# Kernel tuning notes

Hardware: AMD Instinct MI355X
Metric: run time of the kernel (lower is better)

The kernel has to match this reference:

```python
import jax, jax.numpy as jnp
import numpy as np

POOLED_H = 7
POOLED_W = 7
SAMPLING_RATIO = 2


def setup_inputs() -> dict:
    key = jax.random.key(0)
    k1, k2, k3, k4 = jax.random.split(key, 4)
    B, C, H, W = 2, 256, 192, 192
    N = 1024
    stride = 16
    img_h, img_w = H * stride, W * stride
    feature = jax.random.normal(k1, (B, C, H, W), dtype=jnp.float32)
    # well-formed rois: (batch_idx, x1, y1, x2, y2) in image coordinates
    bidx = jax.random.randint(k2, (N, 1), 0, B).astype(jnp.float32)
    p1 = jax.random.uniform(k3, (N, 2), minval=0.0, maxval=0.7)
    wh = jax.random.uniform(k4, (N, 2), minval=0.02, maxval=0.3)
    x1y1 = p1 * jnp.array([img_w, img_h], jnp.float32)
    x2y2 = jnp.minimum(x1y1 + wh * jnp.array([img_w, img_h], jnp.float32),
                       jnp.array([img_w - 1.0, img_h - 1.0], jnp.float32))
    rois = jnp.concatenate([bidx, x1y1[:, :1], x1y1[:, 1:], x2y2[:, :1], x2y2[:, 1:]], axis=1)
    return {"rois": rois, "feature": feature, "stride": stride}


def _roi_align(feature, rois, pooled_h, pooled_w, spatial_scale, ratio):
    B, C, H, W = feature.shape
    N = rois.shape[0]
    b = rois[:, 0].astype(jnp.int32)                     # [N]
    x1 = rois[:, 1] * spatial_scale
    y1 = rois[:, 2] * spatial_scale
    x2 = rois[:, 3] * spatial_scale
    y2 = rois[:, 4] * spatial_scale
    roi_w = jnp.maximum(x2 - x1, 1.0)                    # classic (non-aligned) RoIAlign
    roi_h = jnp.maximum(y2 - y1, 1.0)
    bin_w = roi_w / pooled_w
    bin_h = roi_h / pooled_h

    Sy, Sx = pooled_h * ratio, pooled_w * ratio
    iy = (jnp.arange(Sy, dtype=feature.dtype) + 0.5) / ratio  # in units of bin_h
    ix = (jnp.arange(Sx, dtype=feature.dtype) + 0.5) / ratio
    y = y1[:, None] + iy[None, :] * bin_h[:, None]       # [N, Sy]
    x = x1[:, None] + ix[None, :] * bin_w[:, None]       # [N, Sx]

    def interp_axis(c, size):
        valid = (c > -1.0) & (c < size)
        cc = jnp.clip(c, 0.0, size - 1)
        lo = jnp.floor(cc).astype(jnp.int32)
        lo = jnp.minimum(lo, size - 1)
        hi = jnp.minimum(lo + 1, size - 1)
        frac = cc - lo.astype(c.dtype)
        return valid, lo, hi, frac

    vy, y0, y1i, fy = interp_axis(y, H)
    vx, x0, x1i, fx = interp_axis(x, W)

    hy, ly = (1.0 - fy), fy                              # [N, Sy]
    hx, lx = (1.0 - fx), fx                              # [N, Sx]

    bI = b[:, None, None]

    def gather(yi, xi):
        # -> [N, Sy, Sx, C]
        return feature[bI, :, yi[:, :, None], xi[:, None, :]]

    val = (hy[:, :, None] * hx[:, None, :])[..., None] * gather(y0, x0) \
        + (hy[:, :, None] * lx[:, None, :])[..., None] * gather(y0, x1i) \
        + (ly[:, :, None] * hx[:, None, :])[..., None] * gather(y1i, x0) \
        + (ly[:, :, None] * lx[:, None, :])[..., None] * gather(y1i, x1i)
    val = val * (vy[:, :, None] & vx[:, None, :])[..., None].astype(val.dtype)

    # average sampling grid within each bin
    out = val.reshape(N, pooled_h, ratio, pooled_w, ratio, C).mean(axis=(2, 4))
    return out.transpose(0, 3, 1, 2)                     # [N, C, pooled_h, pooled_w]


def reference(rois, feature, stride):
    rois = rois[:, :5].astype(feature.dtype)
    spatial_scale = 1.0 / stride
    return _roi_align(feature, rois, POOLED_H, POOLED_W, spatial_scale, SAMPLING_RATIO)
```

## Files before the change

kernel.cpp:

```cpp
#include <hip/hip_runtime.h>
#include <hip/hip_fp16.h>

#define POOLED 7
#define RATIO 2

constexpr int C_ = 256;
constexpr int H_ = 192;
constexpr int W_ = 192;
constexpr int P_ = H_ * W_;
constexpr int PP2 = POOLED * POOLED;

constexpr int TC = 32;
constexpr int TP = 128;
constexpr int TPAD = TP + 1;

__global__ __launch_bounds__(256)
void nchw_to_nhwc_h(const float* __restrict__ in, __half* __restrict__ outT) {
    __shared__ float tile[TC][TPAD];
    const int b  = blockIdx.z;
    const int p0 = blockIdx.x * TP;
    const int c0 = blockIdx.y * TC;
    const float* src = in   + (size_t)b * C_ * P_;
    __half*      dst = outT + (size_t)b * P_ * C_;

    const int t = threadIdx.x;

    #pragma unroll
    for (int k = 0; k < 4; ++k) {
        const int q  = t + 256 * k;
        const int c  = q >> 5;
        const int pv = q & 31;
        const float4 v = *(const float4*)&src[(size_t)(c0 + c) * P_ + p0 + 4 * pv];
        tile[c][4 * pv + 0] = v.x;
        tile[c][4 * pv + 1] = v.y;
        tile[c][4 * pv + 2] = v.z;
        tile[c][4 * pv + 3] = v.w;
    }
    __syncthreads();

    #pragma unroll
    for (int k = 0; k < 2; ++k) {
        const int q  = t + 256 * k;
        const int p  = q >> 2;
        const int c8 = (q & 3) * 8;
        union { __half h[8]; float4 f; } u;
        #pragma unroll
        for (int i = 0; i < 8; ++i) u.h[i] = __float2half(tile[c8 + i][p]);
        *(float4*)&dst[(size_t)(p0 + p) * C_ + c0 + c8] = u.f;
    }
}

__global__ __launch_bounds__(512)
void roi_align_nhwc_h(const float* __restrict__ rois,
                      const __half* __restrict__ featT,
                      const int* __restrict__ stride_ptr,
                      float* __restrict__ out, int N) {
    constexpr int BSTRIDE = C_ + 2;
    __shared__ __half lds_out[PP2 * BSTRIDE];
    __shared__ int4 coord[28];

    const int n    = blockIdx.x;
    const int t    = threadIdx.x;
    const int lane = t & 63;
    const int wave = t >> 6;

    const float scale = 1.0f / (float)stride_ptr[0];
    const float* r = rois + (size_t)n * 5;
    const int   b   = (int)r[0];
    const float rx1 = r[1] * scale;
    const float ry1 = r[2] * scale;
    const float rx2 = r[3] * scale;
    const float ry2 = r[4] * scale;
    const float bin_w = fmaxf(rx2 - rx1, 1.0f) * (1.0f / (float)POOLED);
    const float bin_h = fmaxf(ry2 - ry1, 1.0f) * (1.0f / (float)POOLED);

    if (t < 28) {
        const bool  isY   = t < 14;
        const int   s     = isY ? t : t - 14;
        const float start = isY ? ry1 : rx1;
        const float bsz   = isY ? bin_h : bin_w;
        const int   size  = isY ? H_ : W_;
        const float cc0   = start + ((float)s + 0.5f) * 0.5f * bsz;
        const bool  valid = (cc0 > -1.0f) && (cc0 < (float)size);
        float cc = fminf(fmaxf(cc0, 0.0f), (float)(size - 1));
        int lo = (int)floorf(cc);
        if (lo > size - 1) lo = size - 1;
        const int hi = min(lo + 1, size - 1);
        const float frac = (cc - (float)lo) * 0.5f;
        int4 e;
        e.x = isY ? lo * W_ : lo;
        e.y = isY ? hi * W_ : hi;
        e.z = __float_as_int(frac);
        e.w = valid ? 1 : 0;
        coord[t] = e;
    }
    __syncthreads();

    const uint2* fbase = (const uint2*)featT + (size_t)b * P_ * (C_ / 4);
    const int cb = lane * 4;

    for (int bin = wave; bin < PP2; bin += 8) {
        const int ph = bin / POOLED;
        const int pw = bin - ph * POOLED;

        const int4 cxA = coord[14 + 2 * pw];
        const int4 cxB = coord[14 + 2 * pw + 1];

        __half2 acc01 = __float2half2_rn(0.f);
        __half2 acc23 = __float2half2_rn(0.f);

        #pragma unroll
        for (int sy = 0; sy < RATIO; ++sy) {
            const int4  cy = coord[2 * ph + sy];
            const float fy = __int_as_float(cy.z);
            const float hy = 0.5f - fy;

            #pragma unroll
            for (int sx = 0; sx < RATIO; ++sx) {
                const int4 cx = sx ? cxB : cxA;
                if (!(cy.w & cx.w)) continue;
                const float fx = __int_as_float(cx.z);
                const float hx = 0.5f - fx;

                const __half2 W00 = __float2half2_rn(hy * hx);
                const __half2 W01 = __float2half2_rn(hy * fx);
                const __half2 W10 = __float2half2_rn(fy * hx);
                const __half2 W11 = __float2half2_rn(fy * fx);

                const int p00 = cy.x + cx.x;
                const int p01 = cy.x + cx.y;
                const int p10 = cy.y + cx.x;
                const int p11 = cy.y + cx.y;

                const uint2 r00 = fbase[(size_t)p00 * (C_ / 4) + lane];
                const uint2 r01 = fbase[(size_t)p01 * (C_ / 4) + lane];
                const uint2 r10 = fbase[(size_t)p10 * (C_ / 4) + lane];
                const uint2 r11 = fbase[(size_t)p11 * (C_ / 4) + lane];

                acc01 = __hfma2(W00, *(const __half2*)&r00.x, acc01);
                acc23 = __hfma2(W00, *(const __half2*)&r00.y, acc23);
                acc01 = __hfma2(W01, *(const __half2*)&r01.x, acc01);
                acc23 = __hfma2(W01, *(const __half2*)&r01.y, acc23);
                acc01 = __hfma2(W10, *(const __half2*)&r10.x, acc01);
                acc23 = __hfma2(W10, *(const __half2*)&r10.y, acc23);
                acc01 = __hfma2(W11, *(const __half2*)&r11.x, acc01);
                acc23 = __hfma2(W11, *(const __half2*)&r11.y, acc23);
            }
        }

        __half2* dst = (__half2*)&lds_out[bin * BSTRIDE + cb];
        dst[0] = acc01;
        dst[1] = acc23;
    }

    __syncthreads();

    float4* o4 = (float4*)(out + (size_t)n * (C_ * PP2));
    for (int i = t; i < (C_ * PP2) / 4; i += 512) {
        const int l0 = i * 4;
        float4 v;
        #pragma unroll
        for (int j = 0; j < 4; ++j) {
            const int l  = l0 + j;
            const int c  = l / PP2;
            const int bn = l - c * PP2;
            ((float*)&v)[j] = __half2float(lds_out[bn * BSTRIDE + c]);
        }
        o4[i] = v;
    }
}

__global__ __launch_bounds__(256)
void roi_align_kernel(const float* __restrict__ rois,
                      const float* __restrict__ feat,
                      const int* __restrict__ stride_ptr,
                      int B, int C, int H, int W, int N,
                      float* __restrict__ out) {
    const int total = N * C * POOLED * POOLED;
    int idx = blockIdx.x * blockDim.x + threadIdx.x;
    if (idx >= total) return;

    const float scale = 1.0f / (float)stride_ptr[0];

    int pw = idx % POOLED;
    int ph = (idx / POOLED) % POOLED;
    int c  = (idx / (POOLED * POOLED)) % C;
    int n  = idx / (POOLED * POOLED * C);

    const float* r = rois + (size_t)n * 5;
    int b = (int)r[0];
    float x1 = r[1] * scale;
    float y1 = r[2] * scale;
    float x2 = r[3] * scale;
    float y2 = r[4] * scale;
    float bin_w = fmaxf(x2 - x1, 1.0f) / (float)POOLED;
    float bin_h = fmaxf(y2 - y1, 1.0f) / (float)POOLED;

    const float* plane = feat + ((size_t)b * C + c) * (size_t)(H * W);

    float acc = 0.0f;
    #pragma unroll
    for (int sy = 0; sy < RATIO; ++sy) {
        float iy = ((float)(ph * RATIO + sy) + 0.5f) / (float)RATIO;
        float yy = y1 + iy * bin_h;
        bool vy = (yy > -1.0f) && (yy < (float)H);
        float cy = fminf(fmaxf(yy, 0.0f), (float)(H - 1));
        int y0 = (int)floorf(cy);
        if (y0 > H - 1) y0 = H - 1;
        int y1i = min(y0 + 1, H - 1);
        float fy = cy - (float)y0;
        float hy = 1.0f - fy;

        #pragma unroll
        for (int sx = 0; sx < RATIO; ++sx) {
            float ix = ((float)(pw * RATIO + sx) + 0.5f) / (float)RATIO;
            float xx = x1 + ix * bin_w;
            bool vx = (xx > -1.0f) && (xx < (float)W);
            if (!(vy && vx)) continue;
            float cx = fminf(fmaxf(xx, 0.0f), (float)(W - 1));
            int x0 = (int)floorf(cx);
            if (x0 > W - 1) x0 = W - 1;
            int x1i = min(x0 + 1, W - 1);
            float fx = cx - (float)x0;
            float hx = 1.0f - fx;

            float v00 = plane[y0  * W + x0 ];
            float v01 = plane[y0  * W + x1i];
            float v10 = plane[y1i * W + x0 ];
            float v11 = plane[y1i * W + x1i];

            acc += hy * hx * v00 + hy * fx * v01 + fy * hx * v10 + fy * fx * v11;
        }
    }

    out[idx] = acc * 0.25f;
}

extern "C" void kernel_launch(void* const* d_in, const int* in_sizes, int n_in,
                              void* d_out, int out_size, void* d_ws, size_t ws_size,
                              hipStream_t stream) {
    const float* rois = (const float*)d_in[0];
    const float* feat = (const float*)d_in[1];
    const int* stride_ptr = (const int*)d_in[2];

    const int N = in_sizes[0] / 5;
    const int B = in_sizes[1] / (C_ * P_);
    float* out = (float*)d_out;

    const size_t need = (size_t)B * P_ * C_ * sizeof(__half);
    if (ws_size >= need) {
        __half* featT = (__half*)d_ws;
        dim3 tgrid(P_ / TP, C_ / TC, B);
        nchw_to_nhwc_h<<<tgrid, 256, 0, stream>>>(feat, featT);

        roi_align_nhwc_h<<<N, 512, 0, stream>>>(rois, featT, stride_ptr, out, N);
    } else {
        const int total = N * C_ * POOLED * POOLED;
        const int block = 256;
        const int grid = (total + block - 1) / block;
        roi_align_kernel<<<grid, block, 0, stream>>>(rois, feat, stride_ptr,
                                                     B, C_, H_, W_, N, out);
    }
}
```

Before: 165.6 us.

## Split RoIAlign across channel quarters with lane-parallel sample gathers and shuffle reduction

The RoI kernel now launches four 256-thread blocks per RoI, each owning a 64-channel slice, instead of one 512-thread block per RoI. Within a wave, the 8 lane groups each fetch one of the 8 bilinear corner/sample-x combinations as 16-byte loads, and the results are combined with xor-shuffles across groups. Each wave covers a contiguous range of bins and software-pipelines the next bin's loads ahead of the current bin's compute. The goal is more blocks for occupancy, wider memory transactions and better latency hiding, at the cost of shuffle-reduction work and only 8 lanes writing per bin.

```diff
diff --git a/kernel.cpp b/kernel.cpp
--- a/kernel.cpp
+++ b/kernel.cpp
@@ -50,16 +50,21 @@
     }
 }
 
-__global__ __launch_bounds__(512)
+constexpr int CB  = 64;
+constexpr int BPR = C_ / CB;
+constexpr int BST = CB + 2;
+
+__global__ __launch_bounds__(256, 8)
 void roi_align_nhwc_h(const float* __restrict__ rois,
                       const __half* __restrict__ featT,
                       const int* __restrict__ stride_ptr,
                       float* __restrict__ out, int N) {
-    constexpr int BSTRIDE = C_ + 2;
-    __shared__ __half lds_out[PP2 * BSTRIDE];
+    __shared__ __half lds_out[PP2 * BST];
     __shared__ int4 coord[28];
 
-    const int n    = blockIdx.x;
+    const int blk  = blockIdx.x;
+    const int n    = blk >> 2;
+    const int cq   = blk & 3;
     const int t    = threadIdx.x;
     const int lane = t & 63;
     const int wave = t >> 6;
@@ -96,67 +101,89 @@
     }
     __syncthreads();
 
-    const uint2* fbase = (const uint2*)featT + (size_t)b * P_ * (C_ / 4);
-    const int cb = lane * 4;
-
-    for (int bin = wave; bin < PP2; bin += 8) {
+    const uint4* fbase = (const uint4*)featT + (size_t)b * P_ * (C_ / 8);
+    const int cl4   = cq * (CB / 8) + (lane & 7);
+    const int g     = lane >> 3;
+    const int sxsel = g >> 2;
+    const int ysel  = (g >> 1) & 1;
+    const int xsel  = g & 1;
+
+    auto mkbin = [&](int bin, int& o0, int& o1, __half2& w0, __half2& w1) {
         const int ph = bin / POOLED;
         const int pw = bin - ph * POOLED;
-
-        const int4 cxA = coord[14 + 2 * pw];
-        const int4 cxB = coord[14 + 2 * pw + 1];
-
-        __half2 acc01 = __float2half2_rn(0.f);
-        __half2 acc23 = __float2half2_rn(0.f);
-
-        #pragma unroll
-        for (int sy = 0; sy < RATIO; ++sy) {
-            const int4  cy = coord[2 * ph + sy];
-            const float fy = __int_as_float(cy.z);
-            const float hy = 0.5f - fy;
-
-            #pragma unroll
-            for (int sx = 0; sx < RATIO; ++sx) {
-                const int4 cx = sx ? cxB : cxA;
-                if (!(cy.w & cx.w)) continue;
-                const float fx = __int_as_float(cx.z);
-                const float hx = 0.5f - fx;
-
-                const __half2 W00 = __float2half2_rn(hy * hx);
-                const __half2 W01 = __float2half2_rn(hy * fx);
-                const __half2 W10 = __float2half2_rn(fy * hx);
-                const __half2 W11 = __float2half2_rn(fy * fx);
-
-                const int p00 = cy.x + cx.x;
-                const int p01 = cy.x + cx.y;
-                const int p10 = cy.y + cx.x;
-                const int p11 = cy.y + cx.y;
-
-                const uint2 r00 = fbase[(size_t)p00 * (C_ / 4) + lane];
-                const uint2 r01 = fbase[(size_t)p01 * (C_ / 4) + lane];
-                const uint2 r10 = fbase[(size_t)p10 * (C_ / 4) + lane];
-                const uint2 r11 = fbase[(size_t)p11 * (C_ / 4) + lane];
-
-                acc01 = __hfma2(W00, *(const __half2*)&r00.x, acc01);
-                acc23 = __hfma2(W00, *(const __half2*)&r00.y, acc23);
-                acc01 = __hfma2(W01, *(const __half2*)&r01.x, acc01);
-                acc23 = __hfma2(W01, *(const __half2*)&r01.y, acc23);
-                acc01 = __hfma2(W10, *(const __half2*)&r10.x, acc01);
-                acc23 = __hfma2(W10, *(const __half2*)&r10.y, acc23);
-                acc01 = __hfma2(W11, *(const __half2*)&r11.x, acc01);
-                acc23 = __hfma2(W11, *(const __half2*)&r11.y, acc23);
-            }
-        }
-
-        __half2* dst = (__half2*)&lds_out[bin * BSTRIDE + cb];
-        dst[0] = acc01;
-        dst[1] = acc23;
-    }
+        const int4  cx  = coord[14 + 2 * pw + sxsel];
+        const float fx  = __int_as_float(cx.z);
+        const float wx  = xsel ? fx : 0.5f - fx;
+        const int   col = xsel ? cx.y : cx.x;
+
+        const int4  cy0  = coord[2 * ph + 0];
+        const float fy0  = __int_as_float(cy0.z);
+        float wf0 = (ysel ? fy0 : 0.5f - fy0) * wx;
+        if (!(cy0.w & cx.w)) wf0 = 0.0f;
+        o0 = ((ysel ? cy0.y : cy0.x) + col) * (C_ / 8) + cl4;
+        w0 = __float2half2_rn(wf0);
+
+        const int4  cy1  = coord[2 * ph + 1];
+        const float fy1  = __int_as_float(cy1.z);
+        float wf1 = (ysel ? fy1 : 0.5f - fy1) * wx;
+        if (!(cy1.w & cx.w)) wf1 = 0.0f;
+        o1 = ((ysel ? cy1.y : cy1.x) + col) * (C_ / 8) + cl4;
+        w1 = __float2half2_rn(wf1);
+    };
+
+    auto compute_store = [&](int bin, const uint4& A, const uint4& B,
+                             __half2 W0, __half2 W1) {
+        __half2 a0 = __hmul2(W0, *(const __half2*)&A.x);
+        __half2 a1 = __hmul2(W0, *(const __half2*)&A.y);
+        __half2 a2 = __hmul2(W0, *(const __half2*)&A.z);
+        __half2 a3 = __hmul2(W0, *(const __half2*)&A.w);
+        a0 = __hfma2(W1, *(const __half2*)&B.x, a0);
+        a1 = __hfma2(W1, *(const __half2*)&B.y, a1);
+        a2 = __hfma2(W1, *(const __half2*)&B.z, a2);
+        a3 = __hfma2(W1, *(const __half2*)&B.w, a3);
+
+        union HI { __half2 h; int i; };
+        #pragma unroll
+        for (int d = 8; d <= 32; d <<= 1) {
+            HI u0, u1, u2, u3, s0, s1, s2, s3;
+            u0.h = a0; u1.h = a1; u2.h = a2; u3.h = a3;
+            s0.i = __shfl_xor(u0.i, d, 64);
+            s1.i = __shfl_xor(u1.i, d, 64);
+            s2.i = __shfl_xor(u2.i, d, 64);
+            s3.i = __shfl_xor(u3.i, d, 64);
+            a0 = __hadd2(a0, s0.h);
+            a1 = __hadd2(a1, s1.h);
+            a2 = __hadd2(a2, s2.h);
+            a3 = __hadd2(a3, s3.h);
+        }
+        if (lane < 8) {
+            __half2* dst = (__half2*)&lds_out[bin * BST + lane * 8];
+            dst[0] = a0; dst[1] = a1; dst[2] = a2; dst[3] = a3;
+        }
+    };
+
+    const int bin_lo = (wave * PP2) >> 2;
+    const int bin_hi = ((wave + 1) * PP2) >> 2;
+
+    int o0, o1; __half2 w0, w1;
+    mkbin(bin_lo, o0, o1, w0, w1);
+    uint4 vA = fbase[(unsigned)o0];
+    uint4 vB = fbase[(unsigned)o1];
+
+    for (int bin = bin_lo; bin < bin_hi - 1; ++bin) {
+        int no0, no1; __half2 nw0, nw1;
+        mkbin(bin + 1, no0, no1, nw0, nw1);
+        const uint4 pA = fbase[(unsigned)no0];
+        const uint4 pB = fbase[(unsigned)no1];
+        compute_store(bin, vA, vB, w0, w1);
+        vA = pA; vB = pB; w0 = nw0; w1 = nw1;
+    }
+    compute_store(bin_hi - 1, vA, vB, w0, w1);
 
     __syncthreads();
 
-    float4* o4 = (float4*)(out + (size_t)n * (C_ * PP2));
-    for (int i = t; i < (C_ * PP2) / 4; i += 512) {
+    float4* o4 = (float4*)(out + (size_t)n * (C_ * PP2) + (size_t)cq * (CB * PP2));
+    for (int i = t; i < (CB * PP2) / 4; i += 256) {
         const int l0 = i * 4;
         float4 v;
         #pragma unroll
@@ -164,7 +191,7 @@
             const int l  = l0 + j;
             const int c  = l / PP2;
             const int bn = l - c * PP2;
-            ((float*)&v)[j] = __half2float(lds_out[bn * BSTRIDE + c]);
+            ((float*)&v)[j] = __half2float(lds_out[bn * BST + c]);
         }
         o4[i] = v;
     }
@@ -253,7 +280,7 @@
         dim3 tgrid(P_ / TP, C_ / TC, B);
         nchw_to_nhwc_h<<<tgrid, 256, 0, stream>>>(feat, featT);
 
-        roi_align_nhwc_h<<<N, 512, 0, stream>>>(rois, featT, stride_ptr, out, N);
+        roi_align_nhwc_h<<<N * BPR, 256, 0, stream>>>(rois, featT, stride_ptr, out, N);
     } else {
         const int total = N * C_ * POOLED * POOLED;
         const int block = 256;
```

Result: no change. 164.7 us (-0.5%).

## Split RoI channels across two blocks and batch all 16 gathers per bin

Applied to the files above, without the earlier changes.

Each RoI is now handled by two 256-thread blocks, each covering 128 channels. Every lane owns one half2 pair of channels, and each wave processes a contiguous range of bins. Inside a bin, all 16 bilinear corner addresses and weights are computed first, the invalid-sample branch is replaced by a zero mask, and the 16 loads are issued back to back before the FMAs. The aim is more memory-level parallelism and better occupancy with less LDS per block, at the cost of narrower 4-byte loads per lane and redundant coordinate setup for each half-RoI.

```diff
diff --git a/kernel.cpp b/kernel.cpp
--- a/kernel.cpp
+++ b/kernel.cpp
@@ -50,16 +50,21 @@
     }
 }
 
-__global__ __launch_bounds__(512)
+constexpr int CB  = 128;
+constexpr int BPR = C_ / CB;
+constexpr int BST = CB + 2;
+
+__global__ __launch_bounds__(256, 4)
 void roi_align_nhwc_h(const float* __restrict__ rois,
                       const __half* __restrict__ featT,
                       const int* __restrict__ stride_ptr,
                       float* __restrict__ out, int N) {
-    constexpr int BSTRIDE = C_ + 2;
-    __shared__ __half lds_out[PP2 * BSTRIDE];
+    __shared__ __half lds_out[PP2 * BST];
     __shared__ int4 coord[28];
 
-    const int n    = blockIdx.x;
+    const int blk  = blockIdx.x;
+    const int n    = blk >> 1;
+    const int ch0  = (blk & 1) * CB;
     const int t    = threadIdx.x;
     const int lane = t & 63;
     const int wave = t >> 6;
@@ -96,67 +101,73 @@
     }
     __syncthreads();
 
-    const uint2* fbase = (const uint2*)featT + (size_t)b * P_ * (C_ / 4);
-    const int cb = lane * 4;
-
-    for (int bin = wave; bin < PP2; bin += 8) {
+    const uint* fb = (const uint*)featT + (size_t)b * P_ * (C_ / 2)
+                                        + (ch0 >> 1) + lane;
+
+    const int bin_lo = (wave * PP2) >> 2;
+    const int bin_hi = ((wave + 1) * PP2) >> 2;
+
+    for (int bin = bin_lo; bin < bin_hi; ++bin) {
         const int ph = bin / POOLED;
         const int pw = bin - ph * POOLED;
 
-        const int4 cxA = coord[14 + 2 * pw];
-        const int4 cxB = coord[14 + 2 * pw + 1];
-
-        __half2 acc01 = __float2half2_rn(0.f);
-        __half2 acc23 = __float2half2_rn(0.f);
-
-        #pragma unroll
-        for (int sy = 0; sy < RATIO; ++sy) {
-            const int4  cy = coord[2 * ph + sy];
-            const float fy = __int_as_float(cy.z);
-            const float hy = 0.5f - fy;
-
-            #pragma unroll
-            for (int sx = 0; sx < RATIO; ++sx) {
-                const int4 cx = sx ? cxB : cxA;
-                if (!(cy.w & cx.w)) continue;
-                const float fx = __int_as_float(cx.z);
-                const float hx = 0.5f - fx;
-
-                const __half2 W00 = __float2half2_rn(hy * hx);
-                const __half2 W01 = __float2half2_rn(hy * fx);
-                const __half2 W10 = __float2half2_rn(fy * hx);
-                const __half2 W11 = __float2half2_rn(fy * fx);
-
-                const int p00 = cy.x + cx.x;
-                const int p01 = cy.x + cx.y;
-                const int p10 = cy.y + cx.x;
-                const int p11 = cy.y + cx.y;
-
-                const uint2 r00 = fbase[(size_t)p00 * (C_ / 4) + lane];
-                const uint2 r01 = fbase[(size_t)p01 * (C_ / 4) + lane];
-                const uint2 r10 = fbase[(size_t)p10 * (C_ / 4) + lane];
-                const uint2 r11 = fbase[(size_t)p11 * (C_ / 4) + lane];
-
-                acc01 = __hfma2(W00, *(const __half2*)&r00.x, acc01);
-                acc23 = __hfma2(W00, *(const __half2*)&r00.y, acc23);
-                acc01 = __hfma2(W01, *(const __half2*)&r01.x, acc01);
-                acc23 = __hfma2(W01, *(const __half2*)&r01.y, acc23);
-                acc01 = __hfma2(W10, *(const __half2*)&r10.x, acc01);
-                acc23 = __hfma2(W10, *(const __half2*)&r10.y, acc23);
-                acc01 = __hfma2(W11, *(const __half2*)&r11.x, acc01);
-                acc23 = __hfma2(W11, *(const __half2*)&r11.y, acc23);
-            }
-        }
-
-        __half2* dst = (__half2*)&lds_out[bin * BSTRIDE + cb];
-        dst[0] = acc01;
-        dst[1] = acc23;
+        const int4 cy0 = coord[2 * ph + 0];
+        const int4 cy1 = coord[2 * ph + 1];
+        const int4 cx0 = coord[14 + 2 * pw + 0];
+        const int4 cx1 = coord[14 + 2 * pw + 1];
+
+        const float fy0 = __int_as_float(cy0.z);
+        const float fy1 = __int_as_float(cy1.z);
+        const float fx0 = __int_as_float(cx0.z);
+        const float fx1 = __int_as_float(cx1.z);
+
+        const float m00 = (cy0.w & cx0.w) ? 1.0f : 0.0f;
+        const float m01 = (cy0.w & cx1.w) ? 1.0f : 0.0f;
+        const float m10 = (cy1.w & cx0.w) ? 1.0f : 0.0f;
+        const float m11 = (cy1.w & cx1.w) ? 1.0f : 0.0f;
+
+        const float wyl0 = 0.5f - fy0, wyh0 = fy0;
+        const float wyl1 = 0.5f - fy1, wyh1 = fy1;
+        const float wxl0 = 0.5f - fx0, wxh0 = fx0;
+        const float wxl1 = 0.5f - fx1, wxh1 = fx1;
+
+        int   pix[16];
+        float wgt[16];
+        pix[ 0] = cy0.x + cx0.x;  wgt[ 0] = wyl0 * wxl0 * m00;
+        pix[ 1] = cy0.x + cx0.y;  wgt[ 1] = wyl0 * wxh0 * m00;
+        pix[ 2] = cy0.y + cx0.x;  wgt[ 2] = wyh0 * wxl0 * m00;
+        pix[ 3] = cy0.y + cx0.y;  wgt[ 3] = wyh0 * wxh0 * m00;
+        pix[ 4] = cy0.x + cx1.x;  wgt[ 4] = wyl0 * wxl1 * m01;
+        pix[ 5] = cy0.x + cx1.y;  wgt[ 5] = wyl0 * wxh1 * m01;
+        pix[ 6] = cy0.y + cx1.x;  wgt[ 6] = wyh0 * wxl1 * m01;
+        pix[ 7] = cy0.y + cx1.y;  wgt[ 7] = wyh0 * wxh1 * m01;
+        pix[ 8] = cy1.x + cx0.x;  wgt[ 8] = wyl1 * wxl0 * m10;
+        pix[ 9] = cy1.x + cx0.y;  wgt[ 9] = wyl1 * wxh0 * m10;
+        pix[10] = cy1.y + cx0.x;  wgt[10] = wyh1 * wxl0 * m10;
+        pix[11] = cy1.y + cx0.y;  wgt[11] = wyh1 * wxh0 * m10;
+        pix[12] = cy1.x + cx1.x;  wgt[12] = wyl1 * wxl1 * m11;
+        pix[13] = cy1.x + cx1.y;  wgt[13] = wyl1 * wxh1 * m11;
+        pix[14] = cy1.y + cx1.x;  wgt[14] = wyh1 * wxl1 * m11;
+        pix[15] = cy1.y + cx1.y;  wgt[15] = wyh1 * wxh1 * m11;
+
+        uint v[16];
+        #pragma unroll
+        for (int k = 0; k < 16; ++k)
+            v[k] = fb[(size_t)pix[k] * (C_ / 2)];
+
+        __half2 acc = __float2half2_rn(0.f);
+        #pragma unroll
+        for (int k = 0; k < 16; ++k)
+            acc = __hfma2(__float2half2_rn(wgt[k]), *(const __half2*)&v[k], acc);
+
+        *(__half2*)&lds_out[bin * BST + 2 * lane] = acc;
     }
 
     __syncthreads();
 
-    float4* o4 = (float4*)(out + (size_t)n * (C_ * PP2));
-    for (int i = t; i < (C_ * PP2) / 4; i += 512) {
+    float* obase = out + (size_t)n * (C_ * PP2) + (size_t)ch0 * PP2;
+    float4* o4 = (float4*)obase;
+    for (int i = t; i < (CB * PP2) / 4; i += 256) {
         const int l0 = i * 4;
         float4 v;
         #pragma unroll
@@ -164,7 +175,7 @@
             const int l  = l0 + j;
             const int c  = l / PP2;
             const int bn = l - c * PP2;
-            ((float*)&v)[j] = __half2float(lds_out[bn * BSTRIDE + c]);
+            ((float*)&v)[j] = __half2float(lds_out[bn * BST + c]);
         }
         o4[i] = v;
     }
@@ -253,7 +264,8 @@
         dim3 tgrid(P_ / TP, C_ / TC, B);
         nchw_to_nhwc_h<<<tgrid, 256, 0, stream>>>(feat, featT);
 
-        roi_align_nhwc_h<<<N, 512, 0, stream>>>(rois, featT, stride_ptr, out, N);
+        roi_align_nhwc_h<<<N * BPR, 256, 0, stream>>>(rois, featT, stride_ptr,
+                                                      out, N);
     } else {
         const int total = N * C_ * POOLED * POOLED;
         const int block = 256;
```

Result: faster. 162.1 us (-2.1%).
